# Performance work log

Hardware: AMD Instinct MI355X
Metric: run time of the kernel (lower is better)

Reference implementation:

```python
import jax, jax.numpy as jnp
import numpy as np

B, S, D = 4, 4096, 2048


def setup_inputs() -> dict:
    key = jax.random.key(0)
    ks = jax.random.split(key, 9)
    std = 1.0 / np.sqrt(D)
    inp = {
        "x": jax.random.normal(ks[0], (B, S, D), dtype=jnp.float32),
        "Wq": jax.random.normal(ks[1], (D, D), dtype=jnp.float32) * std,
        "bq": jnp.zeros((D,), dtype=jnp.float32),
        "Wk": jax.random.normal(ks[2], (D, D), dtype=jnp.float32) * std,
        "bk": jnp.zeros((D,), dtype=jnp.float32),
        "Wv": jax.random.normal(ks[3], (D, D), dtype=jnp.float32) * std,
        "bv": jnp.zeros((D,), dtype=jnp.float32),
        "Wo": jax.random.normal(ks[4], (D, D), dtype=jnp.float32) * std,
        "bo": jnp.zeros((D,), dtype=jnp.float32),
        "num_heads": 16,
        "num_groups": 4,
    }
    return inp


def reference(x, Wq, bq, Wk, bk, Wv, bv, Wo, bo, num_heads, num_groups):
    b, s, d = x.shape
    H = num_heads
    G = num_groups
    hd = d // H  # head_dim

    q = (x @ Wq + bq).reshape(b, s, H, hd)
    k = (x @ Wk + bk).reshape(b, s, H, hd)
    v = (x @ Wv + bv).reshape(b, s, H, hd)

    # GQA head permutation of queries: [B,S,G,H/G,Dh] -> transpose(2,3) -> [B,S,H,Dh]
    q = q.reshape(b, s, G, H // G, hd).transpose(0, 1, 3, 2, 4).reshape(b, s, H, hd)

    # NOTE: faithful to the source, scores are [B,S,H,H] (attention over heads
    # at each token, NOT over sequence positions), since q/k/v stay [B,S,H,Dh].
    scale = 1.0 / jnp.asarray(hd, x.dtype) ** 0.5
    scores = jnp.einsum('bshd,bstd->bsht', q, k) * scale  # [B,S,H,H]
    probs = jax.nn.softmax(scores, axis=-1)
    attn = jnp.einsum('bsht,bstd->bshd', probs, v)  # [B,S,H,Dh]

    out = attn.reshape(b, s, d) @ Wo + bo
    return out
```

## Files before the change

kernel.cpp:

```cpp
#include <hip/hip_runtime.h>
#include <stdint.h>

#define M_DIM 16384
#define D_DIM 2048
#define HEADS 16
#define HDIM 128

typedef __attribute__((ext_vector_type(8))) short bf16x8;
typedef __attribute__((ext_vector_type(4))) float f32x4;

__device__ __forceinline__ unsigned short f2bf(float f) {
  union { float f; uint32_t u; } c; c.f = f;
  uint32_t u = c.u;
  u += 0x7FFFu + ((u >> 16) & 1u);
  return (unsigned short)(u >> 16);
}
__device__ __forceinline__ float bf2f(unsigned short h) {
  union { float f; uint32_t u; } c; c.u = ((uint32_t)h) << 16;
  return c.f;
}

__device__ __forceinline__ void gload_lds16(const unsigned short* g, unsigned short* l) {
  __builtin_amdgcn_global_load_lds(
      (const __attribute__((address_space(1))) void*)g,
      (__attribute__((address_space(3))) void*)l,
      16, 0, 0);
}

__global__ __launch_bounds__(256) void cvt_x_kernel(const float4* __restrict__ in,
                                                    unsigned short* __restrict__ out,
                                                    int n4) {
  int i = blockIdx.x * blockDim.x + threadIdx.x;
  int stride = gridDim.x * blockDim.x;
  for (; i < n4; i += stride) {
    float4 v = in[i];
    ushort4 o;
    o.x = f2bf(v.x); o.y = f2bf(v.y); o.z = f2bf(v.z); o.w = f2bf(v.w);
    ((ushort4*)out)[i] = o;
  }
}

__global__ __launch_bounds__(256) void cvt_wt_kernel(const float* __restrict__ W0,
                                                     const float* __restrict__ W1,
                                                     const float* __restrict__ W2,
                                                     const float* __restrict__ W3,
                                                     unsigned short* __restrict__ Wt) {
  __shared__ float tile[32][33];
  const int z = blockIdx.z;
  const float* W = z == 0 ? W0 : (z == 1 ? W1 : (z == 2 ? W2 : W3));
  unsigned short* dst = Wt + (size_t)z * D_DIM * D_DIM;
  const int tx = threadIdx.x, ty = threadIdx.y;
  const int n0 = blockIdx.x * 32, k0 = blockIdx.y * 32;
  #pragma unroll
  for (int i = 0; i < 4; ++i)
    tile[ty + i * 8][tx] = W[(size_t)(k0 + ty + i * 8) * D_DIM + n0 + tx];
  __syncthreads();
  #pragma unroll
  for (int i = 0; i < 4; ++i)
    dst[(size_t)(n0 + ty + i * 8) * D_DIM + k0 + tx] = f2bf(tile[tx][ty + i * 8]);
}


#define SYNC_MID()                                          \
  do {                                                      \
    __builtin_amdgcn_sched_barrier(0);                      \
    __builtin_amdgcn_s_barrier();                           \
    __builtin_amdgcn_sched_barrier(0);                      \
  } while (0)

#define SYNC_END()                                          \
  do {                                                      \
    __builtin_amdgcn_sched_barrier(0);                      \
    __builtin_amdgcn_s_barrier();                           \
    __builtin_amdgcn_sched_barrier(0);                      \
  } while (0)

#define READ_A(buf, mh, AF)                                               \
  do {                                                                    \
    const char* _ab = (const char*)&lds[buf][0][0];                       \
    _Pragma("unroll") for (int m = 0; m < 4; ++m) {                       \
      _Pragma("unroll") for (int kk = 0; kk < 2; ++kk) {                  \
        AF[m * 2 + kk] = *(const bf16x8*)(_ab +                           \
            (wm * 128 + (mh) * 64 + m * 16 + fr) * 128 +                  \
            (((kk * 4 + lk8) ^ swz) << 4));                               \
      }                                                                   \
    }                                                                     \
  } while (0)

#define READ_B(buf, nh, BF)                                               \
  do {                                                                    \
    const char* _bb = (const char*)&lds[buf][1][0];                       \
    _Pragma("unroll") for (int n = 0; n < 2; ++n) {                       \
      _Pragma("unroll") for (int kk = 0; kk < 2; ++kk) {                  \
        BF[n * 2 + kk] = *(const bf16x8*)(_bb +                           \
            (wn * 64 + (nh) * 32 + n * 16 + fr) * 128 +                   \
            (((kk * 4 + lk8) ^ swz) << 4));                               \
      }                                                                   \
    }                                                                     \
  } while (0)

#define MFMA_Q(mh, nh, AF, BF)                                            \
  do {                                                                    \
    _Pragma("unroll") for (int m = 0; m < 4; ++m) {                       \
      _Pragma("unroll") for (int n = 0; n < 2; ++n) {                     \
        _Pragma("unroll") for (int kk = 0; kk < 2; ++kk) {                \
          acc[(mh) * 4 + m][(nh) * 2 + n] =                               \
              __builtin_amdgcn_mfma_f32_16x16x32_bf16(                    \
                  AF[m * 2 + kk], BF[n * 2 + kk],                         \
                  acc[(mh) * 4 + m][(nh) * 2 + n], 0, 0, 0);              \
        }                                                                 \
      }                                                                   \
    }                                                                     \
  } while (0)

template<bool QKV>
__global__ __launch_bounds__(512, 2) void gemm256_kernel(
    const unsigned short* __restrict__ A,
    const unsigned short* __restrict__ Bt,
    const float* __restrict__ bias0,
    const float* __restrict__ bias1,
    const float* __restrict__ bias2,
    void* __restrict__ outp) {
  constexpr int K = 2048;
  constexpr int NT = 32;
  __shared__ __align__(16) unsigned short lds[2][2][16384];

  const int tid = threadIdx.x;
  const int wave = tid >> 6;
  const int lane = tid & 63;
  const int fr = lane & 15;
  const int lk8 = lane >> 4;
  const int wm = wave >> 2;
  const int wn = wave & 3;
  const int swz = fr & 7;

  const int nwg = gridDim.x;
  const int orig = blockIdx.x;
  const int wg = (orig & 7) * (nwg >> 3) + (orig >> 3);
  const int mi = wg & 63;
  const int ni = wg >> 6;

  const unsigned short* Ag = A + (size_t)(mi * 256) * K;
  const unsigned short* Bg = Bt + (size_t)(ni * 256) * K;
  const int k8s = (lane & 7) ^ (lane >> 3);

  auto stageA = [&](int tt, int half) {
    unsigned short* dst = &lds[tt & 1][0][0];
    #pragma unroll
    for (int j = 0; j < 2; ++j) {
      const int c = wave * 128 + j * 64 + lane;
      const int r = half * 128 + (c >> 3);
      gload_lds16(Ag + (size_t)r * K + tt * 64 + k8s * 8,
                  dst + (size_t)(half * 1024 + c) * 8);
    }
  };
  auto stageB = [&](int tt, int half) {
    unsigned short* dst = &lds[tt & 1][1][0];
    #pragma unroll
    for (int j = 0; j < 2; ++j) {
      const int c = wave * 128 + j * 64 + lane;
      const int r = half * 128 + (c >> 3);
      gload_lds16(Bg + (size_t)r * K + tt * 64 + k8s * 8,
                  dst + (size_t)(half * 1024 + c) * 8);
    }
  };

  f32x4 acc[8][4];
  #pragma unroll
  for (int m = 0; m < 8; ++m)
    #pragma unroll
    for (int n = 0; n < 4; ++n)
      acc[m][n] = (f32x4){0.f, 0.f, 0.f, 0.f};

  stageA(0, 0); stageA(0, 1); stageB(0, 0); stageB(0, 1);
  stageA(1, 0); stageA(1, 1);
  asm volatile("s_waitcnt vmcnt(4)" ::: "memory");
  __builtin_amdgcn_sched_barrier(0);
  __builtin_amdgcn_s_barrier();
  __builtin_amdgcn_sched_barrier(0);

  bf16x8 af0[8], af1[8], bf[4];
  READ_A(0, 0, af0);

  #pragma unroll 1
  for (int t = 0; t < NT; t += 2) {
    stageB(t + 1, 0);
    READ_B(0, 0, bf);
    SYNC_MID();
    __builtin_amdgcn_s_setprio(1);
    MFMA_Q(0, 0, af0, bf);
    READ_A(0, 1, af1);
    __builtin_amdgcn_s_setprio(0);
    SYNC_END();
    stageB(t + 1, 1);
    SYNC_MID();
    __builtin_amdgcn_s_setprio(1);
    MFMA_Q(1, 0, af1, bf);
    __builtin_amdgcn_s_setprio(0);
    SYNC_END();
    if (t + 2 < NT) stageA(t + 2, 0);
    READ_B(0, 1, bf);
    SYNC_MID();
    __builtin_amdgcn_s_setprio(1);
    MFMA_Q(0, 1, af0, bf);
    __builtin_amdgcn_s_setprio(0);
    if (t + 2 < NT) { asm volatile("s_waitcnt vmcnt(2)" ::: "memory"); }
    else            { asm volatile("s_waitcnt vmcnt(0)" ::: "memory"); }
    SYNC_END();
    if (t + 2 < NT) stageA(t + 2, 1);
    SYNC_MID();
    __builtin_amdgcn_s_setprio(1);
    MFMA_Q(1, 1, af1, bf);
    READ_A(1, 0, af0);
    __builtin_amdgcn_s_setprio(0);
    SYNC_END();
    if (t + 2 < NT) stageB(t + 2, 0);
    READ_B(1, 0, bf);
    SYNC_MID();
    __builtin_amdgcn_s_setprio(1);
    MFMA_Q(0, 0, af0, bf);
    READ_A(1, 1, af1);
    __builtin_amdgcn_s_setprio(0);
    SYNC_END();
    if (t + 2 < NT) stageB(t + 2, 1);
    SYNC_MID();
    __builtin_amdgcn_s_setprio(1);
    MFMA_Q(1, 0, af1, bf);
    __builtin_amdgcn_s_setprio(0);
    SYNC_END();
    if (t + 3 < NT) stageA(t + 3, 0);
    READ_B(1, 1, bf);
    SYNC_MID();
    __builtin_amdgcn_s_setprio(1);
    MFMA_Q(0, 1, af0, bf);
    __builtin_amdgcn_s_setprio(0);
    if (t + 2 < NT) { asm volatile("s_waitcnt vmcnt(2)" ::: "memory"); }
    SYNC_END();
    if (t + 3 < NT) stageA(t + 3, 1);
    SYNC_MID();
    __builtin_amdgcn_s_setprio(1);
    MFMA_Q(1, 1, af1, bf);
    if (t + 2 < NT) READ_A(0, 0, af0);
    __builtin_amdgcn_s_setprio(0);
    SYNC_END();
  }

  const int rb = mi * 256 + wm * 128 + (lane >> 4) * 4;
  const int cb = ni * 256 + wn * 64 + fr;
  if constexpr (QKV) {
    const int plane = (ni * 256) >> 11;
    const float* bias = plane == 0 ? bias0 : (plane == 1 ? bias1 : bias2);
    unsigned short* out = (unsigned short*)outp + (size_t)plane * M_DIM * D_DIM;
    #pragma unroll
    for (int n4 = 0; n4 < 4; ++n4) {
      const int col = (cb + n4 * 16) & (D_DIM - 1);
      const float bv = bias[col];
      #pragma unroll
      for (int m8 = 0; m8 < 8; ++m8)
        #pragma unroll
        for (int e = 0; e < 4; ++e)
          out[(size_t)(rb + m8 * 16 + e) * D_DIM + col] = f2bf(acc[m8][n4][e] + bv);
    }
  } else {
    float* out = (float*)outp;
    #pragma unroll
    for (int n4 = 0; n4 < 4; ++n4) {
      const int col = cb + n4 * 16;
      const float bv = bias0[col];
      #pragma unroll
      for (int m8 = 0; m8 < 8; ++m8)
        #pragma unroll
        for (int e = 0; e < 4; ++e)
          out[(size_t)(rb + m8 * 16 + e) * D_DIM + col] = acc[m8][n4][e] + bv;
    }
  }
}

__global__ __launch_bounds__(256) void attn_kernel(const unsigned short* __restrict__ qkv,
                                                   unsigned short* __restrict__ attnb) {
  __shared__ __align__(16) unsigned short kv_s[4][2][HEADS * HDIM];
  const int tid = threadIdx.x;
  const int wave = tid >> 6;
  const int lane = tid & 63;
  const int t = blockIdx.x * 4 + wave;
  const size_t MD = (size_t)M_DIM * D_DIM;

  const bf16x8* kg = (const bf16x8*)(qkv + MD + (size_t)t * D_DIM);
  const bf16x8* vg = (const bf16x8*)(qkv + 2 * MD + (size_t)t * D_DIM);
  bf16x8* ks = (bf16x8*)&kv_s[wave][0][0];
  bf16x8* vs = (bf16x8*)&kv_s[wave][1][0];
  #pragma unroll
  for (int i = 0; i < 4; ++i) {
    ks[i * 64 + lane] = kg[i * 64 + lane];
    vs[i * 64 + lane] = vg[i * 64 + lane];
  }

  const int ih = lane >> 2;
  const int qd = lane & 3;
  const int hsrc = (ih & 3) * 4 + (ih >> 2);
  const unsigned short* qg = qkv + (size_t)t * D_DIM + hsrc * HDIM + qd * 32;
  float qreg[32];
  #pragma unroll
  for (int c = 0; c < 4; ++c) {
    bf16x8 q8 = ((const bf16x8*)qg)[c];
    #pragma unroll
    for (int e = 0; e < 8; ++e) qreg[c * 8 + e] = bf2f((unsigned short)q8[e]);
  }

  __syncthreads();

  float s[16];
  #pragma unroll
  for (int j = 0; j < 16; ++j) {
    float acc = 0.f;
    const bf16x8* kp = (const bf16x8*)&kv_s[wave][0][j * HDIM + qd * 32];
    #pragma unroll
    for (int c = 0; c < 4; ++c) {
      bf16x8 k8 = kp[c];
      #pragma unroll
      for (int e = 0; e < 8; ++e) acc = fmaf(qreg[c * 8 + e], bf2f((unsigned short)k8[e]), acc);
    }
    acc += __shfl_xor(acc, 1);
    acc += __shfl_xor(acc, 2);
    s[j] = acc * 0.08838834764831845f;
  }

  float mx = s[0];
  #pragma unroll
  for (int j = 1; j < 16; ++j) mx = fmaxf(mx, s[j]);
  float sum = 0.f;
  #pragma unroll
  for (int j = 0; j < 16; ++j) { s[j] = __expf(s[j] - mx); sum += s[j]; }
  const float inv = 1.f / sum;

  float o[32];
  #pragma unroll
  for (int c = 0; c < 32; ++c) o[c] = 0.f;
  #pragma unroll
  for (int j = 0; j < 16; ++j) {
    const float p = s[j] * inv;
    const bf16x8* vp = (const bf16x8*)&kv_s[wave][1][j * HDIM + qd * 32];
    #pragma unroll
    for (int c = 0; c < 4; ++c) {
      bf16x8 v8 = vp[c];
      #pragma unroll
      for (int e = 0; e < 8; ++e) o[c * 8 + e] = fmaf(p, bf2f((unsigned short)v8[e]), o[c * 8 + e]);
    }
  }

  unsigned short* op = attnb + (size_t)t * D_DIM + ih * HDIM + qd * 32;
  #pragma unroll
  for (int c = 0; c < 4; ++c) {
    bf16x8 ov;
    #pragma unroll
    for (int e = 0; e < 8; ++e) ov[e] = (short)f2bf(o[c * 8 + e]);
    ((bf16x8*)op)[c] = ov;
  }
}

extern "C" void kernel_launch(void* const* d_in, const int* in_sizes, int n_in,
                              void* d_out, int out_size, void* d_ws, size_t ws_size,
                              hipStream_t stream) {
  const float* x  = (const float*)d_in[0];
  const float* Wq = (const float*)d_in[1];
  const float* bq = (const float*)d_in[2];
  const float* Wk = (const float*)d_in[3];
  const float* bk = (const float*)d_in[4];
  const float* Wv = (const float*)d_in[5];
  const float* bv = (const float*)d_in[6];
  const float* Wo = (const float*)d_in[7];
  const float* bo = (const float*)d_in[8];

  const size_t MD = (size_t)M_DIM * D_DIM;
  const size_t DD = (size_t)D_DIM * D_DIM;

  unsigned short* xb   = (unsigned short*)d_ws;
  unsigned short* Wt   = xb + MD;
  unsigned short* qkvb = Wt + 4 * DD;
  const size_t need_bytes = (MD + 4 * DD + 3 * MD) * sizeof(unsigned short);
  if (ws_size < need_bytes) return;

  cvt_x_kernel<<<2048, 256, 0, stream>>>((const float4*)x, xb, (int)(MD / 4));

  cvt_wt_kernel<<<dim3(64, 64, 4), dim3(32, 8), 0, stream>>>(Wq, Wk, Wv, Wo, Wt);

  gemm256_kernel<true><<<64 * 24, 512, 0, stream>>>(xb, Wt, bq, bk, bv, qkvb);

  attn_kernel<<<4096, 256, 0, stream>>>(qkvb, xb);

  gemm256_kernel<false><<<64 * 8, 512, 0, stream>>>(xb, Wt + 3 * DD, bo, nullptr, nullptr, d_out);
}
```

Measured before the change: 640.5 us.

## Restructure GEMM main loop into k-half phases with full A fragment preload

The inner loop of the 256x256 GEMM is reorganised from eight quarter-tile phases, which alternated A/B fragment halves, into four k-half phases. Each phase loads all 16 A fragments per buffer up front, reads four B fragments per k-slice, and issues 32 MFMAs at a time. Global-to-LDS staging is batched in pairs, and the vmcnt waits are adjusted to match. The aim is fewer barriers and longer uninterrupted MFMA bursts. The cost is more live registers for A fragments, which could hurt occupancy at launch_bounds(512,2), and less interleaving of LDS reads with compute.

```diff
diff --git a/kernel.cpp b/kernel.cpp
--- a/kernel.cpp
+++ b/kernel.cpp
@@ -87,28 +87,22 @@
     }                                                                     \
   } while (0)
 
-#define READ_B(buf, nh, BF)                                               \
+#define READ_B4(buf, kk)                                                  \
   do {                                                                    \
     const char* _bb = (const char*)&lds[buf][1][0];                       \
-    _Pragma("unroll") for (int n = 0; n < 2; ++n) {                       \
-      _Pragma("unroll") for (int kk = 0; kk < 2; ++kk) {                  \
-        BF[n * 2 + kk] = *(const bf16x8*)(_bb +                           \
-            (wn * 64 + (nh) * 32 + n * 16 + fr) * 128 +                   \
-            (((kk * 4 + lk8) ^ swz) << 4));                               \
-      }                                                                   \
+    _Pragma("unroll") for (int n = 0; n < 4; ++n) {                       \
+      bf[n] = *(const bf16x8*)(_bb +                                      \
+          (wn * 64 + n * 16 + fr) * 128 +                                 \
+          ((((kk) * 4 + lk8) ^ swz) << 4));                               \
     }                                                                     \
   } while (0)
 
-#define MFMA_Q(mh, nh, AF, BF)                                            \
+#define MFMA_HALF(kk)                                                     \
   do {                                                                    \
-    _Pragma("unroll") for (int m = 0; m < 4; ++m) {                       \
-      _Pragma("unroll") for (int n = 0; n < 2; ++n) {                     \
-        _Pragma("unroll") for (int kk = 0; kk < 2; ++kk) {                \
-          acc[(mh) * 4 + m][(nh) * 2 + n] =                               \
-              __builtin_amdgcn_mfma_f32_16x16x32_bf16(                    \
-                  AF[m * 2 + kk], BF[n * 2 + kk],                         \
-                  acc[(mh) * 4 + m][(nh) * 2 + n], 0, 0, 0);              \
-        }                                                                 \
+    _Pragma("unroll") for (int mm = 0; mm < 8; ++mm) {                    \
+      _Pragma("unroll") for (int n = 0; n < 4; ++n) {                     \
+        acc[mm][n] = __builtin_amdgcn_mfma_f32_16x16x32_bf16(             \
+            af[mm * 2 + (kk)], bf[n], acc[mm][n], 0, 0, 0);               \
       }                                                                   \
     }                                                                     \
   } while (0)
@@ -179,69 +173,42 @@
   __builtin_amdgcn_s_barrier();
   __builtin_amdgcn_sched_barrier(0);
 
-  bf16x8 af0[8], af1[8], bf[4];
-  READ_A(0, 0, af0);
+  bf16x8 af[16], bf[4];
 
   #pragma unroll 1
   for (int t = 0; t < NT; t += 2) {
-    stageB(t + 1, 0);
-    READ_B(0, 0, bf);
+    stageB(t + 1, 0); stageB(t + 1, 1);
+    READ_A(0, 0, (af + 0)); READ_A(0, 1, (af + 8));
+    READ_B4(0, 0);
     SYNC_MID();
     __builtin_amdgcn_s_setprio(1);
-    MFMA_Q(0, 0, af0, bf);
-    READ_A(0, 1, af1);
+    MFMA_HALF(0);
     __builtin_amdgcn_s_setprio(0);
     SYNC_END();
-    stageB(t + 1, 1);
+    if (t + 2 < NT) { stageA(t + 2, 0); stageA(t + 2, 1); }
+    READ_B4(0, 1);
     SYNC_MID();
     __builtin_amdgcn_s_setprio(1);
-    MFMA_Q(1, 0, af1, bf);
+    MFMA_HALF(1);
+    __builtin_amdgcn_s_setprio(0);
+    if (t + 2 < NT) { asm volatile("s_waitcnt vmcnt(4)" ::: "memory"); }
+    else            { asm volatile("s_waitcnt vmcnt(0)" ::: "memory"); }
+    SYNC_END();
+    if (t + 2 < NT) { stageB(t + 2, 0); stageB(t + 2, 1); }
+    READ_A(1, 0, (af + 0)); READ_A(1, 1, (af + 8));
+    READ_B4(1, 0);
+    SYNC_MID();
+    __builtin_amdgcn_s_setprio(1);
+    MFMA_HALF(0);
     __builtin_amdgcn_s_setprio(0);
     SYNC_END();
-    if (t + 2 < NT) stageA(t + 2, 0);
-    READ_B(0, 1, bf);
+    if (t + 3 < NT) { stageA(t + 3, 0); stageA(t + 3, 1); }
+    READ_B4(1, 1);
     SYNC_MID();
     __builtin_amdgcn_s_setprio(1);
-    MFMA_Q(0, 1, af0, bf);
+    MFMA_HALF(1);
     __builtin_amdgcn_s_setprio(0);
-    if (t + 2 < NT) { asm volatile("s_waitcnt vmcnt(2)" ::: "memory"); }
-    else            { asm volatile("s_waitcnt vmcnt(0)" ::: "memory"); }
-    SYNC_END();
-    if (t + 2 < NT) stageA(t + 2, 1);
-    SYNC_MID();
-    __builtin_amdgcn_s_setprio(1);
-    MFMA_Q(1, 1, af1, bf);
-    READ_A(1, 0, af0);
-    __builtin_amdgcn_s_setprio(0);
-    SYNC_END();
-    if (t + 2 < NT) stageB(t + 2, 0);
-    READ_B(1, 0, bf);
-    SYNC_MID();
-    __builtin_amdgcn_s_setprio(1);
-    MFMA_Q(0, 0, af0, bf);
-    READ_A(1, 1, af1);
-    __builtin_amdgcn_s_setprio(0);
-    SYNC_END();
-    if (t + 2 < NT) stageB(t + 2, 1);
-    SYNC_MID();
-    __builtin_amdgcn_s_setprio(1);
-    MFMA_Q(1, 0, af1, bf);
-    __builtin_amdgcn_s_setprio(0);
-    SYNC_END();
-    if (t + 3 < NT) stageA(t + 3, 0);
-    READ_B(1, 1, bf);
-    SYNC_MID();
-    __builtin_amdgcn_s_setprio(1);
-    MFMA_Q(0, 1, af0, bf);
-    __builtin_amdgcn_s_setprio(0);
-    if (t + 2 < NT) { asm volatile("s_waitcnt vmcnt(2)" ::: "memory"); }
-    SYNC_END();
-    if (t + 3 < NT) stageA(t + 3, 1);
-    SYNC_MID();
-    __builtin_amdgcn_s_setprio(1);
-    MFMA_Q(1, 1, af1, bf);
-    if (t + 2 < NT) READ_A(0, 0, af0);
-    __builtin_amdgcn_s_setprio(0);
+    if (t + 2 < NT) { asm volatile("s_waitcnt vmcnt(4)" ::: "memory"); }
     SYNC_END();
   }
 
```

Result: slower. 1.280 ms (+99.8%).
